# Optimization experiments

Hardware: AMD Instinct MI355X
Metric: run time of the kernel (lower is better)

Reference implementation:

```python
import jax, jax.numpy as jnp
import numpy as np

B, S, HID = 16, 1024, 768
H, DH = 12, HID // 12


def setup_inputs() -> dict:
    key = jax.random.key(0)
    ks = jax.random.split(key, 10)
    scale = 1.0 / np.sqrt(HID)
    return {
        "hidden_states": jax.random.normal(ks[0], (B, S, HID), jnp.float32),
        "Wq": jax.random.normal(ks[1], (HID, HID), jnp.float32) * scale,
        "bq": jnp.zeros((HID,), jnp.float32),
        "Wk": jax.random.normal(ks[2], (HID, HID), jnp.float32) * scale,
        "bk": jnp.zeros((HID,), jnp.float32),
        "Wv": jax.random.normal(ks[3], (HID, HID), jnp.float32) * scale,
        "bv": jnp.zeros((HID,), jnp.float32),
        # torch init is zeros; use small randn so the linear-attention correction term is exercised
        "phi_k": jax.random.normal(ks[4], (1, H, DH, 1), jnp.float32) * 0.02,
        "phi_kv": jax.random.normal(ks[5], (1, H, DH, DH), jnp.float32) * 0.02,
    }


def _heads(x):
    # [B,S,HID] -> [B,H,S,DH]
    return x.reshape(B, S, H, DH).transpose(0, 2, 1, 3)


def reference(hidden_states, Wq, bq, Wk, bk, Wv, bv, phi_k, phi_kv):
    q = _heads(hidden_states @ Wq.T + bq)
    k = _heads(hidden_states @ Wk.T + bk)
    v = _heads(hidden_states @ Wv.T + bv)

    # phi(x) = ELU(x / d^0.25) + 1   (dropout disabled: eval-mode reference)
    phi_q = jax.nn.elu(q / jnp.asarray(DH, jnp.float32) ** 0.25) + 1.0

    # full softmax-style attention scores with max-subtract
    A = jnp.einsum("bhsd,bhtd->bhst", q, k) / jnp.sqrt(jnp.asarray(DH, jnp.float32))
    max_A = jnp.max(A, axis=-1, keepdims=True)          # [B,H,S,1]
    exp_max_A = jnp.exp(max_A)
    A = jnp.exp(A - max_A)                              # [B,H,S,S]

    # custom normalizer: softmax mass + linear-attention correction
    D = jnp.sum(A, axis=-1, keepdims=True) + jnp.matmul(phi_q, jnp.abs(phi_k)) / exp_max_A

    ctx = (jnp.matmul(A, v) + jnp.matmul(phi_q, phi_kv) / exp_max_A) / D  # [B,H,S,DH]
    out = ctx.transpose(0, 2, 1, 3).reshape(B, S, HID)
    return out
```

## Files before the change

### kernel.cpp

```cpp
#include <hip/hip_runtime.h>
#include <cstdint>
#include <cstddef>

typedef _Float16 f16x8 __attribute__((ext_vector_type(8)));
typedef _Float16 f16x4 __attribute__((ext_vector_type(4)));
typedef float    f32x4 __attribute__((ext_vector_type(4)));
typedef unsigned u32;
typedef const u32 __attribute__((address_space(1)))* gas_ptr;
typedef u32 __attribute__((address_space(3)))* las_ptr;

#define MFMA16(a, b, c) __builtin_amdgcn_mfma_f32_16x16x32_f16((a), (b), (c), 0, 0, 0)

static constexpr int Bb   = 16;
static constexpr int Ss   = 1024;
static constexpr int HID  = 768;
static constexpr int Hh   = 12;
static constexpr int DH   = 64;
static constexpr int Mrows = Bb * Ss;
static constexpr int N3    = 3 * HID;

static constexpr float QSCL  = 0.125f * 1.44269504088896f;
static constexpr float PHSCL = 1.9605161f;

__global__ void cast_f32_to_f16(const float* __restrict__ x, _Float16* __restrict__ y, int n4) {
    int i = blockIdx.x * 256 + threadIdx.x;
    if (i < n4) {
        float4 v = ((const float4*)x)[i];
        f16x4 o;
        o[0] = (_Float16)v.x; o[1] = (_Float16)v.y;
        o[2] = (_Float16)v.z; o[3] = (_Float16)v.w;
        ((f16x4*)y)[i] = o;
    }
}

__global__ void pack_w(const float* __restrict__ Wq, const float* __restrict__ Wk,
                       const float* __restrict__ Wv, const float* __restrict__ bq,
                       const float* __restrict__ bk, const float* __restrict__ bv,
                       _Float16* __restrict__ Wt, float* __restrict__ bias) {
    int i = blockIdx.x * 256 + threadIdx.x;
    if (i < N3) {
        int wsel = i / HID, j = i - wsel * HID;
        bias[i] = (wsel == 0) ? bq[j] : (wsel == 1) ? bk[j] : bv[j];
    }
    if (i < N3 * HID) {
        int n = i / HID, k = i - n * HID;
        int sel = n / HID;
        int nn  = n - sel * HID;
        const float* W = (sel == 0) ? Wq : (sel == 1) ? Wk : Wv;
        Wt[i] = (_Float16)W[nn * HID + k];
    }
}

__global__ __launch_bounds__(256, 2) void qkv_gemm(
    const _Float16* __restrict__ A, const _Float16* __restrict__ Bt,
    const float* __restrict__ bias,
    _Float16* __restrict__ Qo, _Float16* __restrict__ Ko, _Float16* __restrict__ VTo) {
    __shared__ _Float16 As[128 * 32];
    __shared__ _Float16 Bs[128 * 32];
    const int tid  = threadIdx.x;
    const int lane = tid & 63, wid = tid >> 6;
    const int g = lane >> 4, c = lane & 15;
    const int bm = blockIdx.x & 127, bn = blockIdx.x >> 7;
    const int m0 = bm * 128, n0 = bn * 128;
    const int wm = wid >> 1, wn = wid & 1;

    f32x4 acc[4][4] = {};

    for (int kt = 0; kt < HID; kt += 32) {
        if (kt) __syncthreads();
#pragma unroll
        for (int i = 0; i < 2; ++i) {
            int ch  = i * 256 + wid * 64 + lane;
            int row = ch >> 2;
            int kh  = ((ch & 3) ^ ((row >> 1) & 3)) << 3;
            __builtin_amdgcn_global_load_lds(
                (gas_ptr)(A + (size_t)(m0 + row) * HID + kt + kh),
                (las_ptr)(As + (i * 256 + wid * 64) * 8), 16, 0, 0);
            __builtin_amdgcn_global_load_lds(
                (gas_ptr)(Bt + (size_t)(n0 + row) * HID + kt + kh),
                (las_ptr)(Bs + (i * 256 + wid * 64) * 8), 16, 0, 0);
        }
        __syncthreads();

        f16x8 af[4], bf[4];
#pragma unroll
        for (int mi = 0; mi < 4; ++mi) {
            const int row = wm * 64 + mi * 16 + c;
            af[mi] = *(const f16x8*)((const char*)As + row * 64 + ((g ^ ((row >> 1) & 3)) << 4));
        }
#pragma unroll
        for (int ni = 0; ni < 4; ++ni) {
            const int row = wn * 64 + ni * 16 + c;
            bf[ni] = *(const f16x8*)((const char*)Bs + row * 64 + ((g ^ ((row >> 1) & 3)) << 4));
        }
#pragma unroll
        for (int mi = 0; mi < 4; ++mi)
#pragma unroll
            for (int ni = 0; ni < 4; ++ni)
                acc[mi][ni] = MFMA16(af[mi], bf[ni], acc[mi][ni]);
    }

#pragma unroll
    for (int ni = 0; ni < 4; ++ni) {
        const int col    = n0 + wn * 64 + ni * 16 + c;
        const int which  = col / HID;
        const int within = col - which * HID;
        const int hh = within >> 6, d = within & 63;
        const float bias_v = bias[col];
        const float scl = (which == 0) ? QSCL : 1.0f;
#pragma unroll
        for (int mi = 0; mi < 4; ++mi) {
            const int rowg0 = m0 + wm * 64 + mi * 16 + g * 4;
            const int bidx = rowg0 >> 10, s0 = rowg0 & 1023;
            const int bh   = bidx * Hh + hh;
            f16x4 hv4;
#pragma unroll
            for (int r = 0; r < 4; ++r)
                hv4[r] = (_Float16)((acc[mi][ni][r] + bias_v) * scl);
            if (which == 2) {
                const int base64 = (m0 + wm * 64) & 1023;
                const int p = 32 * (mi >> 1) + 8 * g + 4 * (mi & 1);
                *(uint2*)(VTo + ((size_t)bh * DH + d) * Ss + base64 + p) = __builtin_bit_cast(uint2, hv4);
            } else if (which == 0) {
#pragma unroll
                for (int r = 0; r < 4; ++r)
                    Qo[((size_t)bh * Ss + s0 + r) * DH + d] = hv4[r];
            } else {
#pragma unroll
                for (int r = 0; r < 4; ++r)
                    Ko[((size_t)bh * Ss + s0 + r) * DH + d] = hv4[r];
            }
        }
    }
}

__global__ __launch_bounds__(256) void attn_kernel(
    const _Float16* __restrict__ Q, const _Float16* __restrict__ K,
    const _Float16* __restrict__ VT, const float* __restrict__ phi_k,
    const float* __restrict__ phi_kv, float* __restrict__ out) {
    __shared__ _Float16 Kb[2][64 * 64];
    __shared__ _Float16 Vb[2][64 * 64];

    const int tid  = threadIdx.x;
    const int lane = tid & 63, w = tid >> 6;
    const int g = lane >> 4, c = lane & 15;

    const int wg = (blockIdx.x & 7) * 192 + (blockIdx.x >> 3);
    const int bh = wg >> 3, qt = wg & 7;
    const int b = bh / Hh, h = bh - b * Hh;
    const size_t base = (size_t)bh * Ss * DH;
    const _Float16* Kg = K + base;
    const _Float16* Vg = VT + base;

    const int srow = lane >> 3;
    const int scol = (((lane & 7) ^ srow) << 4) >> 1;
    const int sw = (c & 7) << 4;

    const _Float16* Qp = Q + base + (size_t)(qt * 128 + w * 32 + c) * DH + g * 8;
    f16x8 aq[2][2];
    aq[0][0] = *(const f16x8*)(Qp);
    aq[0][1] = *(const f16x8*)(Qp + 32);
    aq[1][0] = *(const f16x8*)(Qp + 16 * DH);
    aq[1][1] = *(const f16x8*)(Qp + 16 * DH + 32);

    float part[2] = {0.f, 0.f};
    f32x4 acco[2][4] = {};

    auto stage = [&](int bf, int t0) {
#pragma unroll
        for (int i = 0; i < 2; ++i) {
            const int row0 = w * 16 + i * 8;
            __builtin_amdgcn_global_load_lds(
                (gas_ptr)(Kg + (size_t)(t0 + row0 + srow) * DH + scol),
                (las_ptr)(&Kb[bf][row0 * 64]), 16, 0, 0);
            __builtin_amdgcn_global_load_lds(
                (gas_ptr)(Vg + (size_t)(row0 + srow) * Ss + t0 + scol),
                (las_ptr)(&Vb[bf][row0 * 64]), 16, 0, 0);
        }
    };

    stage(0, 0);
    __syncthreads();

    for (int t0 = 0; t0 < Ss; t0 += 64) {
        const int bf = (t0 >> 6) & 1;
        if (t0 + 64 < Ss) stage(bf ^ 1, t0 + 64);

        f32x4 z[2][4];
#pragma unroll
        for (int nt = 0; nt < 4; ++nt) {
            const char* kb = (const char*)&Kb[bf][0] + (nt * 16 + c) * 128;
            f16x8 bk0 = *(const f16x8*)(kb + ((g * 16) ^ sw));
            f16x8 bk1 = *(const f16x8*)(kb + ((64 + g * 16) ^ sw));
            f32x4 z0 = {}, z1 = {};
            z0 = MFMA16(bk0, aq[0][0], z0);
            z0 = MFMA16(bk1, aq[0][1], z0);
            z1 = MFMA16(bk0, aq[1][0], z1);
            z1 = MFMA16(bk1, aq[1][1], z1);
            z[0][nt] = z0;
            z[1][nt] = z1;
        }

        f16x8 pb[2][2];
#pragma unroll
        for (int mb = 0; mb < 2; ++mb) {
#pragma unroll
            for (int kk = 0; kk < 2; ++kk) {
                float e0 = __builtin_amdgcn_exp2f(z[mb][2 * kk][0]);
                float e1 = __builtin_amdgcn_exp2f(z[mb][2 * kk][1]);
                float e2 = __builtin_amdgcn_exp2f(z[mb][2 * kk][2]);
                float e3 = __builtin_amdgcn_exp2f(z[mb][2 * kk][3]);
                float e4 = __builtin_amdgcn_exp2f(z[mb][2 * kk + 1][0]);
                float e5 = __builtin_amdgcn_exp2f(z[mb][2 * kk + 1][1]);
                float e6 = __builtin_amdgcn_exp2f(z[mb][2 * kk + 1][2]);
                float e7 = __builtin_amdgcn_exp2f(z[mb][2 * kk + 1][3]);
                part[mb] += (e0 + e1 + e2 + e3) + (e4 + e5 + e6 + e7);
                uint4 pk;
                pk.x = __builtin_bit_cast(u32, __builtin_amdgcn_cvt_pkrtz(e0, e1));
                pk.y = __builtin_bit_cast(u32, __builtin_amdgcn_cvt_pkrtz(e2, e3));
                pk.z = __builtin_bit_cast(u32, __builtin_amdgcn_cvt_pkrtz(e4, e5));
                pk.w = __builtin_bit_cast(u32, __builtin_amdgcn_cvt_pkrtz(e6, e7));
                pb[mb][kk] = __builtin_bit_cast(f16x8, pk);
            }
        }

#pragma unroll
        for (int nd = 0; nd < 4; ++nd) {
            const char* vb = (const char*)&Vb[bf][0] + (nd * 16 + c) * 128;
#pragma unroll
            for (int kk = 0; kk < 2; ++kk) {
                f16x8 va = *(const f16x8*)(vb + ((kk * 64 + g * 16) ^ sw));
                acco[0][nd] = MFMA16(va, pb[0][kk], acco[0][nd]);
                acco[1][nd] = MFMA16(va, pb[1][kk], acco[1][nd]);
            }
        }
        __syncthreads();
    }

    const float* phk = phi_k + h * DH;
    const float* pkv = phi_kv + h * DH * DH;

    f16x8 pq2[2][2];
    float invD[2];
#pragma unroll
    for (int mb = 0; mb < 2; ++mb) {
        const _Float16* Qr = Q + base + (size_t)(qt * 128 + w * 32 + mb * 16 + c) * DH;
        float dot = 0.f;
#pragma unroll
        for (int kk = 0; kk < 2; ++kk) {
            f16x4 qa = *(const f16x4*)(Qr + kk * 32 + 4 * g);
            f16x4 qb = *(const f16x4*)(Qr + kk * 32 + 16 + 4 * g);
            float4 fka = *(const float4*)(phk + kk * 32 + 4 * g);
            float4 fkb = *(const float4*)(phk + kk * 32 + 16 + 4 * g);
            const float fa[4] = {fka.x, fka.y, fka.z, fka.w};
            const float fb[4] = {fkb.x, fkb.y, fkb.z, fkb.w};
            f16x8 pq;
#pragma unroll
            for (int j = 0; j < 4; ++j) {
                float x0 = (float)qa[j] * PHSCL;
                float x1 = (float)qb[j] * PHSCL;
                float p0 = (x0 > 0.f) ? (x0 + 1.f) : __expf(x0);
                float p1 = (x1 > 0.f) ? (x1 + 1.f) : __expf(x1);
                dot += p0 * fabsf(fa[j]) + p1 * fabsf(fb[j]);
                pq[j]     = (_Float16)p0;
                pq[4 + j] = (_Float16)p1;
            }
            pq2[mb][kk] = pq;
        }
        dot += __shfl_xor(dot, 16);
        dot += __shfl_xor(dot, 32);
        float s = part[mb];
        s += __shfl_xor(s, 16);
        s += __shfl_xor(s, 32);
        invD[mb] = 1.f / (s + dot);
    }

#pragma unroll
    for (int nd = 0; nd < 4; ++nd) {
        f16x8 fa[2];
#pragma unroll
        for (int kk = 0; kk < 2; ++kk) {
            f16x8 t;
#pragma unroll
            for (int j = 0; j < 8; ++j) {
                int dh = kk * 32 + 16 * (j >> 2) + 4 * g + (j & 3);
                t[j] = (_Float16)pkv[dh * DH + nd * 16 + c];
            }
            fa[kk] = t;
        }
#pragma unroll
        for (int mb = 0; mb < 2; ++mb) {
            f32x4 cc = {};
            cc = MFMA16(fa[0], pq2[mb][0], cc);
            cc = MFMA16(fa[1], pq2[mb][1], cc);
            f32x4 o = (acco[mb][nd] + cc) * invD[mb];
            const int srow_o = qt * 128 + w * 32 + mb * 16 + c;
            float* op = out + ((size_t)b * Ss + srow_o) * HID + h * DH + nd * 16 + 4 * g;
            *(f32x4*)op = o;
        }
    }
}

extern "C" void kernel_launch(void* const* d_in, const int* in_sizes, int n_in,
                              void* d_out, int out_size, void* d_ws, size_t ws_size,
                              hipStream_t stream) {
    (void)in_sizes; (void)n_in; (void)out_size;
    const float* hs   = (const float*)d_in[0];
    const float* Wq   = (const float*)d_in[1];
    const float* bq   = (const float*)d_in[2];
    const float* Wk   = (const float*)d_in[3];
    const float* bk   = (const float*)d_in[4];
    const float* Wv   = (const float*)d_in[5];
    const float* bv   = (const float*)d_in[6];
    const float* phik = (const float*)d_in[7];
    const float* phikv= (const float*)d_in[8];
    float* out = (float*)d_out;

    char* ws = (char*)d_ws;
    constexpr size_t szA   = (size_t)Mrows * HID * 2;
    constexpr size_t szWt  = (size_t)N3 * HID * 2;
    constexpr size_t szBia = (size_t)N3 * 4;
    constexpr size_t szQ   = (size_t)Bb * Hh * Ss * DH * 2;
    _Float16* A16  = (_Float16*)(ws);
    _Float16* Wt   = (_Float16*)(ws + szA);
    float*    bias = (float*)(ws + szA + szWt);
    _Float16* Qb   = (_Float16*)(ws + szA + szWt + szBia);
    _Float16* Kb   = (_Float16*)(ws + szA + szWt + szBia + szQ);
    _Float16* VTb  = (_Float16*)(ws + szA + szWt + szBia + 2 * szQ);
    (void)ws_size;

    cast_f32_to_f16<<<(Mrows * HID / 4 + 255) / 256, 256, 0, stream>>>(hs, A16, Mrows * HID / 4);
    pack_w<<<(N3 * HID + 255) / 256, 256, 0, stream>>>(Wq, Wk, Wv, bq, bk, bv, Wt, bias);
    qkv_gemm<<<dim3((Mrows / 128) * (N3 / 128)), 256, 0, stream>>>(A16, Wt, bias, Qb, Kb, VTb);
    attn_kernel<<<dim3(Bb * Hh * (Ss / 128)), 256, 0, stream>>>(Qb, Kb, VTb, phik, phikv, out);
}
```

Before: 182.9 us.

## Double-buffer QKV GEMM LDS, fuse prep kernels, add MFMA priority hints

The QKV GEMM moves to two LDS buffers so the next K-slice's global-to-LDS loads are issued while MFMAs run on the current slice, and the leading barrier per iteration is replaced by a trailing one. The cast and weight-pack kernels are merged into a single launch, with the weight pack vectorised to 8 elements per thread. The attention kernel raises wave priority around its MFMA sections with s_setprio. Costs are double the GEMM LDS use, which may lower occupancy, and a bigger prep kernel.

```diff
diff --git a/kernel.cpp b/kernel.cpp
--- a/kernel.cpp
+++ b/kernel.cpp
@@ -22,32 +22,39 @@
 static constexpr float QSCL  = 0.125f * 1.44269504088896f;
 static constexpr float PHSCL = 1.9605161f;
 
-__global__ void cast_f32_to_f16(const float* __restrict__ x, _Float16* __restrict__ y, int n4) {
-    int i = blockIdx.x * 256 + threadIdx.x;
-    if (i < n4) {
-        float4 v = ((const float4*)x)[i];
+__global__ void prep(const float* __restrict__ hs, _Float16* __restrict__ A16,
+                     const float* __restrict__ Wq, const float* __restrict__ Wk,
+                     const float* __restrict__ Wv, const float* __restrict__ bq,
+                     const float* __restrict__ bk, const float* __restrict__ bv,
+                     _Float16* __restrict__ Wt, float* __restrict__ bias) {
+    const int i = blockIdx.x * 256 + threadIdx.x;
+    if (i < Mrows * HID / 4) {
+        float4 v = ((const float4*)hs)[i];
         f16x4 o;
         o[0] = (_Float16)v.x; o[1] = (_Float16)v.y;
         o[2] = (_Float16)v.z; o[3] = (_Float16)v.w;
-        ((f16x4*)y)[i] = o;
-    }
-}
-
-__global__ void pack_w(const float* __restrict__ Wq, const float* __restrict__ Wk,
-                       const float* __restrict__ Wv, const float* __restrict__ bq,
-                       const float* __restrict__ bk, const float* __restrict__ bv,
-                       _Float16* __restrict__ Wt, float* __restrict__ bias) {
-    int i = blockIdx.x * 256 + threadIdx.x;
+        ((f16x4*)A16)[i] = o;
+    }
+    if (i < N3 * HID / 8) {
+        const int i8 = i * 8;
+        int n = i8 / HID;
+        int k = i8 - n * HID;
+        int sel = n / HID;
+        int nn  = n - sel * HID;
+        const float* W = (sel == 0) ? Wq : (sel == 1) ? Wk : Wv;
+        const float* wp = W + (size_t)nn * HID + k;
+        float4 v0 = *(const float4*)wp;
+        float4 v1 = *(const float4*)(wp + 4);
+        uint4 o;
+        o.x = __builtin_bit_cast(u32, __builtin_amdgcn_cvt_pkrtz(v0.x, v0.y));
+        o.y = __builtin_bit_cast(u32, __builtin_amdgcn_cvt_pkrtz(v0.z, v0.w));
+        o.z = __builtin_bit_cast(u32, __builtin_amdgcn_cvt_pkrtz(v1.x, v1.y));
+        o.w = __builtin_bit_cast(u32, __builtin_amdgcn_cvt_pkrtz(v1.z, v1.w));
+        *(uint4*)(Wt + i8) = o;
+    }
     if (i < N3) {
         int wsel = i / HID, j = i - wsel * HID;
         bias[i] = (wsel == 0) ? bq[j] : (wsel == 1) ? bk[j] : bv[j];
-    }
-    if (i < N3 * HID) {
-        int n = i / HID, k = i - n * HID;
-        int sel = n / HID;
-        int nn  = n - sel * HID;
-        const float* W = (sel == 0) ? Wq : (sel == 1) ? Wk : Wv;
-        Wt[i] = (_Float16)W[nn * HID + k];
     }
 }
 
@@ -55,8 +62,8 @@
     const _Float16* __restrict__ A, const _Float16* __restrict__ Bt,
     const float* __restrict__ bias,
     _Float16* __restrict__ Qo, _Float16* __restrict__ Ko, _Float16* __restrict__ VTo) {
-    __shared__ _Float16 As[128 * 32];
-    __shared__ _Float16 Bs[128 * 32];
+    __shared__ _Float16 As[2][128 * 32];
+    __shared__ _Float16 Bs[2][128 * 32];
     const int tid  = threadIdx.x;
     const int lane = tid & 63, wid = tid >> 6;
     const int g = lane >> 4, c = lane & 15;
@@ -66,8 +73,7 @@
 
     f32x4 acc[4][4] = {};
 
-    for (int kt = 0; kt < HID; kt += 32) {
-        if (kt) __syncthreads();
+    auto stage = [&](int bf, int kt) {
 #pragma unroll
         for (int i = 0; i < 2; ++i) {
             int ch  = i * 256 + wid * 64 + lane;
@@ -75,29 +81,38 @@
             int kh  = ((ch & 3) ^ ((row >> 1) & 3)) << 3;
             __builtin_amdgcn_global_load_lds(
                 (gas_ptr)(A + (size_t)(m0 + row) * HID + kt + kh),
-                (las_ptr)(As + (i * 256 + wid * 64) * 8), 16, 0, 0);
+                (las_ptr)(&As[bf][(i * 256 + wid * 64) * 8]), 16, 0, 0);
             __builtin_amdgcn_global_load_lds(
                 (gas_ptr)(Bt + (size_t)(n0 + row) * HID + kt + kh),
-                (las_ptr)(Bs + (i * 256 + wid * 64) * 8), 16, 0, 0);
-        }
-        __syncthreads();
+                (las_ptr)(&Bs[bf][(i * 256 + wid * 64) * 8]), 16, 0, 0);
+        }
+    };
+
+    stage(0, 0);
+    __syncthreads();
+
+    for (int kt = 0; kt < HID; kt += 32) {
+        const int cur = (kt >> 5) & 1;
+        if (kt + 32 < HID) stage(cur ^ 1, kt + 32);
 
         f16x8 af[4], bf[4];
 #pragma unroll
         for (int mi = 0; mi < 4; ++mi) {
             const int row = wm * 64 + mi * 16 + c;
-            af[mi] = *(const f16x8*)((const char*)As + row * 64 + ((g ^ ((row >> 1) & 3)) << 4));
+            af[mi] = *(const f16x8*)((const char*)&As[cur][0] + row * 64 + ((g ^ ((row >> 1) & 3)) << 4));
         }
 #pragma unroll
         for (int ni = 0; ni < 4; ++ni) {
             const int row = wn * 64 + ni * 16 + c;
-            bf[ni] = *(const f16x8*)((const char*)Bs + row * 64 + ((g ^ ((row >> 1) & 3)) << 4));
+            bf[ni] = *(const f16x8*)((const char*)&Bs[cur][0] + row * 64 + ((g ^ ((row >> 1) & 3)) << 4));
         }
 #pragma unroll
         for (int mi = 0; mi < 4; ++mi)
 #pragma unroll
             for (int ni = 0; ni < 4; ++ni)
                 acc[mi][ni] = MFMA16(af[mi], bf[ni], acc[mi][ni]);
+
+        __syncthreads();
     }
 
 #pragma unroll
@@ -187,6 +202,7 @@
         if (t0 + 64 < Ss) stage(bf ^ 1, t0 + 64);
 
         f32x4 z[2][4];
+        __builtin_amdgcn_s_setprio(1);
 #pragma unroll
         for (int nt = 0; nt < 4; ++nt) {
             const char* kb = (const char*)&Kb[bf][0] + (nt * 16 + c) * 128;
@@ -200,6 +216,7 @@
             z[0][nt] = z0;
             z[1][nt] = z1;
         }
+        __builtin_amdgcn_s_setprio(0);
 
         f16x8 pb[2][2];
 #pragma unroll
@@ -224,6 +241,7 @@
             }
         }
 
+        __builtin_amdgcn_s_setprio(1);
 #pragma unroll
         for (int nd = 0; nd < 4; ++nd) {
             const char* vb = (const char*)&Vb[bf][0] + (nd * 16 + c) * 128;
@@ -234,6 +252,7 @@
                 acco[1][nd] = MFMA16(va, pb[1][kk], acco[1][nd]);
             }
         }
+        __builtin_amdgcn_s_setprio(0);
         __syncthreads();
     }
 
@@ -329,8 +348,7 @@
     _Float16* VTb  = (_Float16*)(ws + szA + szWt + szBia + 2 * szQ);
     (void)ws_size;
 
-    cast_f32_to_f16<<<(Mrows * HID / 4 + 255) / 256, 256, 0, stream>>>(hs, A16, Mrows * HID / 4);
-    pack_w<<<(N3 * HID + 255) / 256, 256, 0, stream>>>(Wq, Wk, Wv, bq, bk, bv, Wt, bias);
+    prep<<<(Mrows * HID / 4 + 255) / 256, 256, 0, stream>>>(hs, A16, Wq, Wk, Wv, bq, bk, bv, Wt, bias);
     qkv_gemm<<<dim3((Mrows / 128) * (N3 / 128)), 256, 0, stream>>>(A16, Wt, bias, Qb, Kb, VTb);
     attn_kernel<<<dim3(Bb * Hh * (Ss / 128)), 256, 0, stream>>>(Qb, Kb, VTb, phik, phikv, out);
 }
```

New measurement: 178.2 us. -2.6%, faster.
